# Kernel optimization log

Hardware: AMD Instinct MI355X
Metric: run time of the kernel (lower is better)

## Reference

```python
import jax, jax.numpy as jnp
import numpy as np

H = 512   # hidden_size
L = 2     # decoder_layer
B = 64    # batch
T = 2048  # encoder sequence length


def setup_inputs() -> dict:
    key = jax.random.key(0)
    ks = jax.random.split(key, 9)
    hidden = jax.random.normal(ks[0], (L, B, H), dtype=jnp.float32)
    encoder_output = jax.random.normal(ks[1], (T, B, H), dtype=jnp.float32)
    enc_len = jax.random.randint(ks[2], (B,), T // 2, T + 1, dtype=jnp.int32)
    s = 0.02
    Wh = jax.random.normal(ks[3], (H, H), dtype=jnp.float32) * s  # hidden_proj
    bh = jnp.zeros((H,), dtype=jnp.float32)
    We = jax.random.normal(ks[4], (H, H), dtype=jnp.float32) * s  # encoder_output_proj
    be = jnp.zeros((H,), dtype=jnp.float32)
    Wo = jax.random.normal(ks[5], (H,), dtype=jnp.float32) * s    # out: Linear(H, 1)
    bo = jnp.zeros((1,), dtype=jnp.float32)
    return {"hidden": hidden, "encoder_output": encoder_output, "enc_len": enc_len,
            "Wh": Wh, "bh": bh, "We": We, "be": be, "Wo": Wo, "bo": bo}


def reference(hidden, encoder_output, enc_len, Wh, bh, We, be, Wo, bo):
    # encoder_output: [T,B,H] -> [B,T,H]
    enc = jnp.swapaxes(encoder_output, 0, 1)
    # bmm with (1/L) addMask == mean over decoder layers: [L,B,H] -> [B,H]
    h = jnp.mean(hidden, axis=0)
    hidden_attn = h @ Wh.T + bh                      # [B,H]
    enc_attn = jnp.einsum('bth,oh->bto', enc, We) + be  # [B,T,H]
    res = jnp.tanh(enc_attn + hidden_attn[:, None, :])  # [B,T,H]
    scores = res @ Wo + bo[0]                        # [B,T]
    # per-sample masked softmax over valid prefix [0:enc_len[i])
    mask = jnp.arange(T)[None, :] < enc_len[:, None]  # [B,T]
    neg = jnp.asarray(-jnp.inf, dtype=scores.dtype)
    w = jax.nn.softmax(jnp.where(mask, scores, neg), axis=1)
    w = jnp.where(mask, w, 0.0)
    return w[:, :, None]  # [B,T,1]
```

## Files before the change

### kernel.cpp

```cpp
#include <hip/hip_runtime.h>
#include <stdint.h>


typedef __attribute__((ext_vector_type(4))) float f32x4;
typedef __attribute__((ext_vector_type(8))) __bf16 bf16x8;
typedef __attribute__((ext_vector_type(8))) unsigned short u16x8;

#define AS3 __attribute__((address_space(3)))
#define AS1 __attribute__((address_space(1)))

__device__ __forceinline__ unsigned short f2bf(float f) {
  unsigned u = __builtin_bit_cast(unsigned, f);
  return (unsigned short)((u + 0x7FFFu + ((u >> 16) & 1u)) >> 16);
}

__device__ __forceinline__ float fast_tanh(float x) {
  float t = __expf(-2.0f * __builtin_fabsf(x));
  float r = (1.0f - t) * __builtin_amdgcn_rcpf(1.0f + t);
  return __builtin_copysignf(r, x);
}

#define WAVE_SYNC() do { \
  asm volatile("s_waitcnt lgkmcnt(0)" ::: "memory"); \
  __builtin_amdgcn_s_barrier(); \
  __builtin_amdgcn_sched_barrier(0); \
} while (0)

__global__ void prep_comb_kernel(const float* __restrict__ hidden,
                                 const float* __restrict__ Wh,
                                 const float* __restrict__ bh,
                                 const float* __restrict__ be,
                                 float* __restrict__ comb) {
  __shared__ float hb[512];
  const int b = blockIdx.x, tid = threadIdx.x;
  for (int i = tid; i < 512; i += 256)
    hb[i] = 0.5f * (hidden[b * 512 + i] + hidden[32768 + b * 512 + i]);
  __syncthreads();
  for (int o = tid; o < 512; o += 256) {
    const f32x4* wr = (const f32x4*)(Wh + o * 512);
    const f32x4* hv = (const f32x4*)hb;
    float s = 0.f;
    for (int k = 0; k < 128; ++k) {
      f32x4 w = wr[k], x = hv[k];
      s += w.x * x.x + w.y * x.y + w.z * x.z + w.w * x.w;
    }
    comb[b * 512 + o] = s + bh[o] + be[o];
  }
}

__global__ void prep_pack_kernel(const float* __restrict__ We,
                                 unsigned short* __restrict__ wsw) {
  const int gid = blockIdx.x * 256 + threadIdx.x;
  const int s = gid >> 11;
  const int rem = gid & 2047;
  const int o = rem >> 2;
  const int g = rem & 3;
  const float* src = We + o * 512 + s * 32 + g * 8;
  u16x8 p;
#pragma unroll
  for (int e = 0; e < 8; ++e) p[e] = f2bf(src[e]);
  const int dgran = s * 2048 + o * 4 + ((g ^ (o >> 1)) & 3);
  *(u16x8*)(wsw + (long)dgran * 8) = p;
}

__global__ __launch_bounds__(512, 2) void gemm_score_kernel(
    const float* __restrict__ enc,
    const unsigned short* __restrict__ wsw,
    const float* __restrict__ comb,
    const float* __restrict__ Wo,
    float* __restrict__ scores)
{
  __shared__ __align__(16) unsigned char Blds[3][32768];
  __shared__ __align__(16) unsigned char Alds[2][8192];
  __shared__ float spart[4][128];

  const int tid = threadIdx.x;
  const int lane = tid & 63;
  const int wave = tid >> 6;
  const int wm = wave >> 2;
  const int wn = wave & 3;
  const int l15 = lane & 15;
  const int lq = lane >> 4;

  const long r0 = (long)blockIdx.x * 128;

  const int arow = tid >> 2;
  const int ag = tid & 3;
  const float* aglb = enc + (r0 + arow) * 512 + ag * 8;
  const unsigned awoff = (unsigned)(arow * 64 + (((ag ^ (arow >> 1)) & 3) << 4));

  const unsigned char* bglb = (const unsigned char*)wsw + (long)tid * 16;

  const unsigned swz = (unsigned)(((lq ^ (l15 >> 1)) & 3) << 4);
  const unsigned aoff = (unsigned)((wm * 64 + l15) * 64) + swz;
  const unsigned boff = (unsigned)((wn * 128 + l15) * 64) + swz;

  f32x4 acc[4][8];
#pragma unroll
  for (int m = 0; m < 4; ++m)
#pragma unroll
    for (int j = 0; j < 8; ++j) acc[m][j] = (f32x4){0.f, 0.f, 0.f, 0.f};

  f32x4 apre[2][2];

#pragma unroll
  for (int c = 0; c < 4; ++c)
    __builtin_amdgcn_global_load_lds((const AS1 unsigned int*)(bglb + c * 8192),
                                     (AS3 unsigned int*)(&Blds[0][tid * 16 + c * 8192]),
                                     16, 0, 0);
  apre[0][0] = *(const f32x4*)(aglb);
  apre[0][1] = *(const f32x4*)(aglb + 4);
#pragma unroll
  for (int c = 0; c < 4; ++c)
    __builtin_amdgcn_global_load_lds((const AS1 unsigned int*)(bglb + 32768 + c * 8192),
                                     (AS3 unsigned int*)(&Blds[1][tid * 16 + c * 8192]),
                                     16, 0, 0);
  apre[1][0] = *(const f32x4*)(aglb + 32);
  apre[1][1] = *(const f32x4*)(aglb + 32 + 4);
  {
    u16x8 p;
    p[0] = f2bf(apre[0][0].x); p[1] = f2bf(apre[0][0].y);
    p[2] = f2bf(apre[0][0].z); p[3] = f2bf(apre[0][0].w);
    p[4] = f2bf(apre[0][1].x); p[5] = f2bf(apre[0][1].y);
    p[6] = f2bf(apre[0][1].z); p[7] = f2bf(apre[0][1].w);
    *(u16x8*)(&Alds[0][awoff]) = p;
  }
  WAVE_SYNC();

#pragma unroll
  for (int ks = 0; ks < 16; ++ks) {
    if (ks + 2 < 16) {
      const unsigned char* bs = bglb + (long)(ks + 2) * 32768;
      unsigned char* bd = &Blds[(ks + 2) % 3][tid * 16];
#pragma unroll
      for (int c = 0; c < 4; ++c)
        __builtin_amdgcn_global_load_lds((const AS1 unsigned int*)(bs + c * 8192),
                                         (AS3 unsigned int*)(bd + c * 8192),
                                         16, 0, 0);
      apre[ks & 1][0] = *(const f32x4*)(aglb + (ks + 2) * 32);
      apre[ks & 1][1] = *(const f32x4*)(aglb + (ks + 2) * 32 + 4);
    }
    __builtin_amdgcn_sched_barrier(0);

    bf16x8 af[4];
#pragma unroll
    for (int m = 0; m < 4; ++m)
      af[m] = *(const bf16x8*)(&Alds[ks & 1][aoff + m * 1024]);
#pragma unroll
    for (int jn = 0; jn < 8; ++jn) {
      bf16x8 bf = *(const bf16x8*)(&Blds[ks % 3][boff + jn * 1024]);
#pragma unroll
      for (int m = 0; m < 4; ++m)
        acc[m][jn] = __builtin_amdgcn_mfma_f32_16x16x32_bf16(af[m], bf, acc[m][jn], 0, 0, 0);
    }

    if (ks < 15) {
      const f32x4* a = apre[(ks + 1) & 1];
      u16x8 p;
      p[0] = f2bf(a[0].x); p[1] = f2bf(a[0].y); p[2] = f2bf(a[0].z); p[3] = f2bf(a[0].w);
      p[4] = f2bf(a[1].x); p[5] = f2bf(a[1].y); p[6] = f2bf(a[1].z); p[7] = f2bf(a[1].w);
      *(u16x8*)(&Alds[(ks + 1) & 1][awoff]) = p;
    }
    WAVE_SYNC();
  }

  float wo[8];
#pragma unroll
  for (int jn = 0; jn < 8; ++jn) wo[jn] = Wo[wn * 128 + jn * 16 + l15];

#pragma unroll
  for (int m = 0; m < 4; ++m) {
#pragma unroll
    for (int q = 0; q < 4; ++q) {
      const int b = m * 16 + lq * 4 + q;
      const float* crow = comb + b * 512;
      float s = 0.f;
#pragma unroll
      for (int jn = 0; jn < 8; ++jn) {
        const int col = wn * 128 + jn * 16 + l15;
        const float x = acc[m][jn][q] + crow[col];
        s += fast_tanh(x) * wo[jn];
      }
      s += __shfl_xor(s, 1, 16);
      s += __shfl_xor(s, 2, 16);
      s += __shfl_xor(s, 4, 16);
      s += __shfl_xor(s, 8, 16);
      if (l15 == 0) spart[wn][wm * 64 + b] = s;
    }
  }
  __syncthreads();
  if (tid < 128) {
    float s = spart[0][tid] + spart[1][tid] + spart[2][tid] + spart[3][tid];
    const int b = tid & 63;
    const long t = (long)blockIdx.x * 2 + (tid >> 6);
    scores[(long)b * 2048 + t] = s;
  }
}

__global__ void softmax_kernel(const float* __restrict__ scores,
                               const int* __restrict__ enc_len,
                               float* __restrict__ out) {
  const int b = blockIdx.x;
  const int tid = threadIdx.x;
  const int lane = tid & 63;
  const int wv = tid >> 6;
  __shared__ float red[4];
  const int n = enc_len[b];
  const float* sc = scores + (long)b * 2048;

  float v[8];
  float m = -1e30f;
#pragma unroll
  for (int j = 0; j < 8; ++j) {
    const int t = tid + j * 256;
    v[j] = sc[t];
    if (t < n) m = fmaxf(m, v[j]);
  }
#pragma unroll
  for (int k = 32; k; k >>= 1) m = fmaxf(m, __shfl_xor(m, k, 64));
  if (lane == 0) red[wv] = m;
  __syncthreads();
  m = fmaxf(fmaxf(red[0], red[1]), fmaxf(red[2], red[3]));
  __syncthreads();

  float s = 0.f;
#pragma unroll
  for (int j = 0; j < 8; ++j) {
    const int t = tid + j * 256;
    const float e = (t < n) ? __expf(v[j] - m) : 0.f;
    v[j] = e;
    s += e;
  }
#pragma unroll
  for (int k = 32; k; k >>= 1) s += __shfl_xor(s, k, 64);
  if (lane == 0) red[wv] = s;
  __syncthreads();
  s = red[0] + red[1] + red[2] + red[3];
  const float inv = 1.0f / s;
#pragma unroll
  for (int j = 0; j < 8; ++j) {
    const int t = tid + j * 256;
    out[(long)b * 2048 + t] = v[j] * inv;
  }
}

extern "C" void kernel_launch(void* const* d_in, const int* in_sizes, int n_in,
                              void* d_out, int out_size, void* d_ws, size_t ws_size,
                              hipStream_t stream) {
  const float* hidden = (const float*)d_in[0];
  const float* enc    = (const float*)d_in[1];
  const int*   enclen = (const int*)d_in[2];
  const float* Wh     = (const float*)d_in[3];
  const float* bh     = (const float*)d_in[4];
  const float* We     = (const float*)d_in[5];
  const float* be     = (const float*)d_in[6];
  const float* Wo     = (const float*)d_in[7];
  float* out = (float*)d_out;

  uint8_t* ws = (uint8_t*)d_ws;
  unsigned short* wsw = (unsigned short*)ws;
  float* comb   = (float*)(ws + 524288);
  float* scores = (float*)(ws + 524288 + 131072);

  hipLaunchKernelGGL(prep_comb_kernel, dim3(64), dim3(256), 0, stream,
                     hidden, Wh, bh, be, comb);
  hipLaunchKernelGGL(prep_pack_kernel, dim3(128), dim3(256), 0, stream, We, wsw);
  hipLaunchKernelGGL(gemm_score_kernel, dim3(1024), dim3(512), 0, stream,
                     enc, wsw, comb, Wo, scores);
  hipLaunchKernelGGL(softmax_kernel, dim3(64), dim3(256), 0, stream,
                     scores, enclen, out);
}
```

Baseline: 152.1 us.

## Deepen GEMM prefetch pipeline to four stages with explicit vmcnt waits

Grows the B shared-memory ring from three to four buffers and prefetches the fp32 encoder A rows four K-steps ahead instead of two. Explicit s_waitcnt vmcnt counts let each iteration wait only for the data it needs, and the A bf16 conversion now happens before the MFMA block rather than after it. MFMA sections run at raised wave priority through s_setprio. The aim is to hide more global-memory latency on the streaming encoder read. The cost is about 146KB of LDS per block and more registers for the deeper A prefetch, and the hand-counted vmcnt values must match the real number of in-flight loads.

Result: no change. 154.0 us (+1.2%).

```diff
diff --git a/kernel.cpp b/kernel.cpp
--- a/kernel.cpp
+++ b/kernel.cpp
@@ -19,6 +19,11 @@
   float r = (1.0f - t) * __builtin_amdgcn_rcpf(1.0f + t);
   return __builtin_copysignf(r, x);
 }
+
+#define VMWAIT(n) do { \
+  asm volatile("s_waitcnt vmcnt(" #n ")" ::: "memory"); \
+  __builtin_amdgcn_sched_barrier(0); \
+} while (0)
 
 #define WAVE_SYNC() do { \
   asm volatile("s_waitcnt lgkmcnt(0)" ::: "memory"); \
@@ -70,7 +75,7 @@
     const float* __restrict__ Wo,
     float* __restrict__ scores)
 {
-  __shared__ __align__(16) unsigned char Blds[3][32768];
+  __shared__ __align__(16) unsigned char Blds[4][32768];
   __shared__ __align__(16) unsigned char Alds[2][8192];
   __shared__ float spart[4][128];
 
@@ -101,66 +106,74 @@
 #pragma unroll
     for (int j = 0; j < 8; ++j) acc[m][j] = (f32x4){0.f, 0.f, 0.f, 0.f};
 
-  f32x4 apre[2][2];
-
-#pragma unroll
-  for (int c = 0; c < 4; ++c)
-    __builtin_amdgcn_global_load_lds((const AS1 unsigned int*)(bglb + c * 8192),
-                                     (AS3 unsigned int*)(&Blds[0][tid * 16 + c * 8192]),
-                                     16, 0, 0);
-  apre[0][0] = *(const f32x4*)(aglb);
-  apre[0][1] = *(const f32x4*)(aglb + 4);
-#pragma unroll
-  for (int c = 0; c < 4; ++c)
-    __builtin_amdgcn_global_load_lds((const AS1 unsigned int*)(bglb + 32768 + c * 8192),
-                                     (AS3 unsigned int*)(&Blds[1][tid * 16 + c * 8192]),
-                                     16, 0, 0);
-  apre[1][0] = *(const f32x4*)(aglb + 32);
-  apre[1][1] = *(const f32x4*)(aglb + 32 + 4);
+  f32x4 apre[4][2];
+
+#pragma unroll
+  for (int s = 0; s < 3; ++s)
+#pragma unroll
+    for (int c = 0; c < 4; ++c)
+      __builtin_amdgcn_global_load_lds(
+          (const AS1 unsigned int*)(bglb + (long)s * 32768 + c * 8192),
+          (AS3 unsigned int*)(&Blds[s][tid * 16 + c * 8192]), 16, 0, 0);
+  f32x4 a00 = *(const f32x4*)(aglb);
+  f32x4 a01 = *(const f32x4*)(aglb + 4);
+#pragma unroll
+  for (int i = 1; i <= 3; ++i) {
+    apre[i][0] = *(const f32x4*)(aglb + i * 32);
+    apre[i][1] = *(const f32x4*)(aglb + i * 32 + 4);
+  }
+  VMWAIT(6);
   {
     u16x8 p;
-    p[0] = f2bf(apre[0][0].x); p[1] = f2bf(apre[0][0].y);
-    p[2] = f2bf(apre[0][0].z); p[3] = f2bf(apre[0][0].w);
-    p[4] = f2bf(apre[0][1].x); p[5] = f2bf(apre[0][1].y);
-    p[6] = f2bf(apre[0][1].z); p[7] = f2bf(apre[0][1].w);
+    p[0] = f2bf(a00.x); p[1] = f2bf(a00.y); p[2] = f2bf(a00.z); p[3] = f2bf(a00.w);
+    p[4] = f2bf(a01.x); p[5] = f2bf(a01.y); p[6] = f2bf(a01.z); p[7] = f2bf(a01.w);
     *(u16x8*)(&Alds[0][awoff]) = p;
   }
   WAVE_SYNC();
 
 #pragma unroll
   for (int ks = 0; ks < 16; ++ks) {
-    if (ks + 2 < 16) {
-      const unsigned char* bs = bglb + (long)(ks + 2) * 32768;
-      unsigned char* bd = &Blds[(ks + 2) % 3][tid * 16];
+    if (ks + 3 < 16) {
+      const unsigned char* bs = bglb + (long)(ks + 3) * 32768;
+      unsigned char* bd = &Blds[(ks + 3) & 3][tid * 16];
 #pragma unroll
       for (int c = 0; c < 4; ++c)
         __builtin_amdgcn_global_load_lds((const AS1 unsigned int*)(bs + c * 8192),
                                          (AS3 unsigned int*)(bd + c * 8192),
                                          16, 0, 0);
-      apre[ks & 1][0] = *(const f32x4*)(aglb + (ks + 2) * 32);
-      apre[ks & 1][1] = *(const f32x4*)(aglb + (ks + 2) * 32 + 4);
+    }
+    if (ks + 4 < 16) {
+      apre[(ks + 4) & 3][0] = *(const f32x4*)(aglb + (ks + 4) * 32);
+      apre[(ks + 4) & 3][1] = *(const f32x4*)(aglb + (ks + 4) * 32 + 4);
     }
     __builtin_amdgcn_sched_barrier(0);
 
-    bf16x8 af[4];
-#pragma unroll
-    for (int m = 0; m < 4; ++m)
-      af[m] = *(const bf16x8*)(&Alds[ks & 1][aoff + m * 1024]);
-#pragma unroll
-    for (int jn = 0; jn < 8; ++jn) {
-      bf16x8 bf = *(const bf16x8*)(&Blds[ks % 3][boff + jn * 1024]);
-#pragma unroll
-      for (int m = 0; m < 4; ++m)
-        acc[m][jn] = __builtin_amdgcn_mfma_f32_16x16x32_bf16(af[m], bf, acc[m][jn], 0, 0, 0);
-    }
-
-    if (ks < 15) {
-      const f32x4* a = apre[(ks + 1) & 1];
+    if (ks <= 12)      VMWAIT(18);
+    else if (ks == 13) VMWAIT(10);
+    else if (ks == 14) VMWAIT(4);
+    else               VMWAIT(0);
+
+    if (ks + 1 < 16) {
+      const f32x4* a = apre[(ks + 1) & 3];
       u16x8 p;
       p[0] = f2bf(a[0].x); p[1] = f2bf(a[0].y); p[2] = f2bf(a[0].z); p[3] = f2bf(a[0].w);
       p[4] = f2bf(a[1].x); p[5] = f2bf(a[1].y); p[6] = f2bf(a[1].z); p[7] = f2bf(a[1].w);
       *(u16x8*)(&Alds[(ks + 1) & 1][awoff]) = p;
     }
+
+    __builtin_amdgcn_s_setprio(1);
+    bf16x8 af[4];
+#pragma unroll
+    for (int m = 0; m < 4; ++m)
+      af[m] = *(const bf16x8*)(&Alds[ks & 1][aoff + m * 1024]);
+#pragma unroll
+    for (int jn = 0; jn < 8; ++jn) {
+      bf16x8 bf = *(const bf16x8*)(&Blds[ks & 3][boff + jn * 1024]);
+#pragma unroll
+      for (int m = 0; m < 4; ++m)
+        acc[m][jn] = __builtin_amdgcn_mfma_f32_16x16x32_bf16(af[m], bf, acc[m][jn], 0, 0, 0);
+    }
+    __builtin_amdgcn_s_setprio(0);
     WAVE_SYNC();
   }
 
```
